# Performance work log

Measured on AMD Instinct MI355X. Metric: run time of the kernel, lower is better.

Reference implementation:

```python
import jax, jax.numpy as jnp
import numpy as np

IN_FEATURES = 128
OUT_FEATURES = 128
GRID_SIZE = 5
SPLINE_ORDER = 3
N_KNOTS = GRID_SIZE + 2 * SPLINE_ORDER + 1  # 12
N_BASIS = GRID_SIZE + SPLINE_ORDER          # 8


def b_spline_basis(x, grid, spline_order):
    # x: [N, in], grid: [in, n_knots] -> basis: [N, in, n_basis]
    xe = x[..., None]
    basis = ((xe >= grid[..., :-1]) & (xe < grid[..., 1:])).astype(x.dtype)
    for k in range(1, spline_order + 1):
        left = (xe - grid[..., :-(k + 1)]) / (grid[..., k:-1] - grid[..., :-(k + 1)] + 1e-08)
        right = (grid[..., k + 1:] - xe) / (grid[..., k + 1:] - grid[..., 1:-k] + 1e-08)
        basis = left * basis[..., :-1] + right * basis[..., 1:]
    return basis


def setup_inputs() -> dict:
    key = jax.random.key(0)
    k_x, k_bw, k_sw = jax.random.split(key, 3)
    x = jax.random.normal(k_x, (16, 4096, IN_FEATURES), dtype=jnp.float32)
    grid = jnp.tile(jnp.linspace(-1.0, 1.0, N_KNOTS, dtype=jnp.float32)[None, :], (IN_FEATURES, 1))
    base_weight = jax.random.normal(k_bw, (OUT_FEATURES, IN_FEATURES), dtype=jnp.float32) * 0.1
    base_bias = jnp.zeros((OUT_FEATURES,), dtype=jnp.float32)
    spline_weight = jax.random.normal(k_sw, (OUT_FEATURES, IN_FEATURES, N_BASIS), dtype=jnp.float32) * 0.1
    spline_bias = jnp.zeros((OUT_FEATURES,), dtype=jnp.float32)
    spline_scale = jnp.ones((1,), dtype=jnp.float32)
    return {"x": x, "grid": grid, "base_weight": base_weight, "base_bias": base_bias,
            "spline_weight": spline_weight, "spline_bias": spline_bias, "spline_scale": spline_scale}


def reference(x, grid, base_weight, base_bias, spline_weight, spline_bias, spline_scale):
    orig_shape = x.shape
    x_flat = x.reshape(-1, IN_FEATURES)                      # [N, in]
    base_out = jax.nn.silu(x_flat) @ base_weight.T + base_bias  # [N, out]
    x_norm = jnp.tanh(x_flat)
    basis = b_spline_basis(x_norm, grid, SPLINE_ORDER)       # [N, in, n_basis]
    spline_out = jnp.einsum('oib,nib->no', spline_weight, basis) + spline_bias
    out = base_out + spline_scale * spline_out
    return out.reshape(*orig_shape[:-1], OUT_FEATURES)
```

## Files before the change

kernel.cpp:

```cpp
#include <hip/hip_runtime.h>
#include <hip/hip_bf16.h>


typedef __attribute__((ext_vector_type(8))) short short8;
typedef __attribute__((ext_vector_type(4))) float f32x4;
typedef __attribute__((ext_vector_type(4))) unsigned int u32x4;
typedef __attribute__((ext_vector_type(8))) unsigned short u16x8;

#define GLOAD_LDS16(g, l) __builtin_amdgcn_global_load_lds(                 \
    (const __attribute__((address_space(1))) void*)(g),                     \
    (__attribute__((address_space(3))) void*)(l), 16, 0, 0)

__device__ __forceinline__ unsigned short f2bf(float f) {
    unsigned u = __builtin_bit_cast(unsigned, f);
    return (unsigned short)((u + 0x7fffu + ((u >> 16) & 1u)) >> 16);
}
__device__ __forceinline__ unsigned pack_bf2(float lo, float hi) {
    unsigned r;
    asm("v_cvt_pk_bf16_f32 %0, %1, %2" : "=v"(r) : "v"(lo), "v"(hi));
    return r;
}
__device__ __forceinline__ float fexp2(float f) { return __builtin_amdgcn_exp2f(f); }
__device__ __forceinline__ float frcp(float f)  { return __builtin_amdgcn_rcpf(f); }
__device__ __forceinline__ float fsilu(float v) {
    return v * frcp(1.0f + fexp2(v * -1.442695041f));
}

__device__ __forceinline__ short8 spline_frag(float xv) {
    const float s6 = 0.16666667f;
    float e  = fexp2(xv * 2.885390082f);
    float r  = frcp(1.0f + e);
    float t  = __builtin_fmaf(-2.0f, r, 1.0f);
    float u  = __builtin_fmaf(t, 5.5f, 5.5f);
    int   j  = (int)u;
    float w  = u - (float)j;
    float w2 = w * w;
    float v0 = __builtin_fmaf(__builtin_fmaf(__builtin_fmaf(-s6, w, 0.5f), w, -0.5f), w, s6);
    float v1 = __builtin_fmaf(__builtin_fmaf(0.5f, w, -1.0f), w2, 0.66666667f);
    float v3 = (w * s6) * w2;
    float v2 = (1.0f - v0) - (v1 + v3);
    unsigned P01 = pack_bf2(v0, v1);
    unsigned P23 = pack_bf2(v2, v3);
    unsigned long long P = (unsigned long long)P01 | ((unsigned long long)P23 << 32);
    int s = (j - 3) << 4;
    unsigned long long lo, hi;
    lo = (s >= 0) ? ((s < 64) ? (P << s) : 0ull) : (P >> (-s));
    hi = (s <= 0) ? 0ull
                  : ((s < 64) ? (P >> (64 - s))
                              : ((s < 128) ? (P << (s - 64)) : 0ull));
    u32x4 f = { (unsigned)lo, (unsigned)(lo >> 32), (unsigned)hi, (unsigned)(hi >> 32) };
    return __builtin_bit_cast(short8, f);
}

__global__ void kan_prep(const float* __restrict__ spline_w,
                         const float* __restrict__ base_w,
                         const float* __restrict__ scale_p,
                         unsigned short* __restrict__ wpre) {
    int g   = blockIdx.x * 256 + threadIdx.x;
    int p   = g >> 11;
    int rem = g & 2047;
    int o   = rem >> 4;
    int k0  = (rem & 15) << 3;
    const float* src = (p < 8) ? (spline_w + (o << 10) + (p << 7) + k0)
                               : (base_w + (o << 7) + k0);
    float s = (p < 8) ? scale_p[0] : 1.0f;
    float4 a = *(const float4*)(src);
    float4 b = *(const float4*)(src + 4);
    u16x8 pk = { f2bf(a.x * s), f2bf(a.y * s), f2bf(a.z * s), f2bf(a.w * s),
                 f2bf(b.x * s), f2bf(b.y * s), f2bf(b.z * s), f2bf(b.w * s) };
    unsigned byte = (unsigned)(((o << 8) + (k0 << 1)) ^ ((o & 7) << 4));
    *(u16x8*)((char*)wpre + (p << 15) + byte) = pk;
}

__global__ __launch_bounds__(256, 2) void kan_main(
    const float* __restrict__ x,
    const unsigned short* __restrict__ wpre,
    const float* __restrict__ base_b,
    const float* __restrict__ spline_b,
    const float* __restrict__ scale_p,
    float* __restrict__ out)
{
    __shared__ unsigned short lds_w[2 * 128 * 128];

    const int tid  = threadIdx.x;
    const int lane = tid & 63;
    const int wave = tid >> 6;
    const int l15  = lane & 15;
    const int kb   = lane >> 4;
    const int row0 = (int)blockIdx.x * 128;

    f32x4 acc[2][8];
#pragma unroll
    for (int m = 0; m < 2; ++m)
#pragma unroll
        for (int n = 0; n < 8; ++n) acc[m][n] = (f32x4){0.f, 0.f, 0.f, 0.f};

    char* lwbase = (char*)lds_w;
    const char* wsrc = (const char*)wpre;

    const float* xp0 = x + (row0 + (wave << 5) + l15) * 128 + kb;
    const float* xp1 = xp0 + 16 * 128;

    {
        const char* src = wsrc + (wave << 13) + (lane << 4);
        char* dst = lwbase + (wave << 13);
#pragma unroll
        for (int it = 0; it < 8; ++it) GLOAD_LDS16(src + (it << 10), dst + (it << 10));
    }
    float xsA[2][4], xsB[2][4];
    float4 xb[2][4][2];
#pragma unroll
    for (int ks = 0; ks < 4; ++ks) { xsA[0][ks] = xp0[ks << 2]; xsA[1][ks] = xp1[ks << 2]; }
    __syncthreads();

#define PHASE(P, XS_CUR, XS_NXT)                                              \
    {                                                                         \
        char* cur = lwbase + (((P) & 1) << 15);                               \
        char* nxt = lwbase + ((((P) + 1) & 1) << 15);                         \
        {                                                                     \
            const char* src = wsrc + (((P) + 1) << 15) + (wave << 13) + (lane << 4); \
            char* dst = nxt + (wave << 13);                                   \
            _Pragma("unroll")                                                 \
            for (int it = 0; it < 8; ++it)                                    \
                GLOAD_LDS16(src + (it << 10), dst + (it << 10));              \
        }                                                                     \
        if ((P) < 7) {                                                        \
            const int c = ((P) + 1) << 4;                                     \
            _Pragma("unroll")                                                 \
            for (int ks = 0; ks < 4; ++ks) {                                  \
                XS_NXT[0][ks] = xp0[c + (ks << 2)];                           \
                XS_NXT[1][ks] = xp1[c + (ks << 2)];                           \
            }                                                                 \
        } else {                                                              \
            const float* xq0 = x + (row0 + (wave << 5) + l15) * 128 + (kb << 3); \
            const float* xq1 = xq0 + 16 * 128;                                \
            _Pragma("unroll")                                                 \
            for (int ks = 0; ks < 4; ++ks) {                                  \
                xb[0][ks][0] = *(const float4*)(xq0 + (ks << 5));             \
                xb[0][ks][1] = *(const float4*)(xq0 + (ks << 5) + 4);         \
                xb[1][ks][0] = *(const float4*)(xq1 + (ks << 5));             \
                xb[1][ks][1] = *(const float4*)(xq1 + (ks << 5) + 4);         \
            }                                                                 \
        }                                                                     \
        short8 af[2][4];                                                      \
        _Pragma("unroll")                                                     \
        for (int m = 0; m < 2; ++m)                                           \
            _Pragma("unroll")                                                 \
            for (int ks = 0; ks < 4; ++ks) af[m][ks] = spline_frag(XS_CUR[m][ks]); \
        _Pragma("unroll")                                                     \
        for (int ks = 0; ks < 4; ++ks) {                                      \
            short8 bfr[8];                                                    \
            _Pragma("unroll")                                                 \
            for (int n = 0; n < 8; ++n) {                                     \
                int o = (n << 4) + l15;                                       \
                unsigned byte = (unsigned)(((o << 8) + (ks << 6) + (kb << 4)) ^ ((o & 7) << 4)); \
                bfr[n] = *(const short8*)(cur + byte);                        \
            }                                                                 \
            _Pragma("unroll")                                                 \
            for (int m = 0; m < 2; ++m)                                       \
                _Pragma("unroll")                                             \
                for (int n = 0; n < 8; ++n)                                   \
                    acc[m][n] = __builtin_amdgcn_mfma_f32_16x16x32_bf16(      \
                        af[m][ks], bfr[n], acc[m][n], 0, 0, 0);               \
        }                                                                     \
        __syncthreads();                                                      \
    }

    PHASE(0, xsA, xsB)
    PHASE(1, xsB, xsA)
    PHASE(2, xsA, xsB)
    PHASE(3, xsB, xsA)
    PHASE(4, xsA, xsB)
    PHASE(5, xsB, xsA)
    PHASE(6, xsA, xsB)
    PHASE(7, xsB, xsA)
#undef PHASE

    {
        char* cur = lwbase;
        short8 af[2][4];
#pragma unroll
        for (int m = 0; m < 2; ++m)
#pragma unroll
            for (int ks = 0; ks < 4; ++ks) {
                float4 a0 = xb[m][ks][0], a1 = xb[m][ks][1];
                u32x4 f = { pack_bf2(fsilu(a0.x), fsilu(a0.y)),
                            pack_bf2(fsilu(a0.z), fsilu(a0.w)),
                            pack_bf2(fsilu(a1.x), fsilu(a1.y)),
                            pack_bf2(fsilu(a1.z), fsilu(a1.w)) };
                af[m][ks] = __builtin_bit_cast(short8, f);
            }
#pragma unroll
        for (int ks = 0; ks < 4; ++ks) {
            short8 bfr[8];
#pragma unroll
            for (int n = 0; n < 8; ++n) {
                int o = (n << 4) + l15;
                unsigned byte = (unsigned)(((o << 8) + (ks << 6) + (kb << 4)) ^ ((o & 7) << 4));
                bfr[n] = *(const short8*)(cur + byte);
            }
#pragma unroll
            for (int m = 0; m < 2; ++m)
#pragma unroll
                for (int n = 0; n < 8; ++n)
                    acc[m][n] = __builtin_amdgcn_mfma_f32_16x16x32_bf16(
                        af[m][ks], bfr[n], acc[m][n], 0, 0, 0);
        }
    }

    const float scale = scale_p[0];
    float* ob = out + (row0 + (wave << 5) + (kb << 2)) * 128 + l15;
#pragma unroll
    for (int n = 0; n < 8; ++n) {
        int o = (n << 4) + l15;
        float bias = base_b[o] + scale * spline_b[o];
#pragma unroll
        for (int m = 0; m < 2; ++m) {
            float* obm = ob + (m << 4) * 128 + (n << 4);
#pragma unroll
            for (int j = 0; j < 4; ++j)
                obm[j * 128] = acc[m][n][j] + bias;
        }
    }
}

extern "C" void kernel_launch(void* const* d_in, const int* in_sizes, int n_in,
                              void* d_out, int out_size, void* d_ws, size_t ws_size,
                              hipStream_t stream) {
    const float* x  = (const float*)d_in[0];
    const float* bw = (const float*)d_in[2];
    const float* bb = (const float*)d_in[3];
    const float* sw = (const float*)d_in[4];
    const float* sb = (const float*)d_in[5];
    const float* sc = (const float*)d_in[6];
    float* out = (float*)d_out;

    unsigned short* wpre = (unsigned short*)d_ws;
    hipLaunchKernelGGL(kan_prep, dim3(72), dim3(256), 0, stream, sw, bw, sc, wpre);

    int nrows   = in_sizes[0] / 128;
    int nblocks = nrows / 128;
    hipLaunchKernelGGL(kan_main, dim3(nblocks), dim3(256), 0, stream,
                       x, wpre, bb, sb, sc, out);
}
```

Baseline: 42.26 us.

## Software-pipeline spline basis computation one phase ahead, interleaved with MFMAs

Computes the A-fragments (spline basis or SiLU) for the next phase while the current phase's MFMAs run, spreading the VALU work between MFMA groups rather than doing it all before them. X loads now run two phases ahead, with a double-buffered fragment array. The goal is to overlap VALU transcendental work with matrix-core execution. In exchange it raises register pressure (two fragment sets plus two x buffers), which could lower occupancy or cause spills.

```diff
diff --git a/kernel.cpp b/kernel.cpp
--- a/kernel.cpp
+++ b/kernel.cpp
@@ -109,11 +109,18 @@
     }
     float xsA[2][4], xsB[2][4];
     float4 xb[2][4][2];
+    short8 afA[2][4], afB[2][4];
 #pragma unroll
     for (int ks = 0; ks < 4; ++ks) { xsA[0][ks] = xp0[ks << 2]; xsA[1][ks] = xp1[ks << 2]; }
+#pragma unroll
+    for (int ks = 0; ks < 4; ++ks) { xsB[0][ks] = xp0[16 + (ks << 2)]; xsB[1][ks] = xp1[16 + (ks << 2)]; }
+#pragma unroll
+    for (int m = 0; m < 2; ++m)
+#pragma unroll
+        for (int ks = 0; ks < 4; ++ks) afA[m][ks] = spline_frag(xsA[m][ks]);
     __syncthreads();
 
-#define PHASE(P, XS_CUR, XS_NXT)                                              \
+#define PHASE(P, XS_CONS, XS_LOAD, AF_CUR, AF_NXT)                            \
     {                                                                         \
         char* cur = lwbase + (((P) & 1) << 15);                               \
         char* nxt = lwbase + ((((P) + 1) & 1) << 15);                         \
@@ -124,14 +131,14 @@
             for (int it = 0; it < 8; ++it)                                    \
                 GLOAD_LDS16(src + (it << 10), dst + (it << 10));              \
         }                                                                     \
-        if ((P) < 7) {                                                        \
-            const int c = ((P) + 1) << 4;                                     \
+        if ((P) < 6) {                                                        \
+            const int c = ((P) + 2) << 4;                                     \
             _Pragma("unroll")                                                 \
             for (int ks = 0; ks < 4; ++ks) {                                  \
-                XS_NXT[0][ks] = xp0[c + (ks << 2)];                           \
-                XS_NXT[1][ks] = xp1[c + (ks << 2)];                           \
-            }                                                                 \
-        } else {                                                              \
+                XS_LOAD[0][ks] = xp0[c + (ks << 2)];                          \
+                XS_LOAD[1][ks] = xp1[c + (ks << 2)];                          \
+            }                                                                 \
+        } else if ((P) == 6) {                                                \
             const float* xq0 = x + (row0 + (wave << 5) + l15) * 128 + (kb << 3); \
             const float* xq1 = xq0 + 16 * 128;                                \
             _Pragma("unroll")                                                 \
@@ -142,11 +149,6 @@
                 xb[1][ks][1] = *(const float4*)(xq1 + (ks << 5) + 4);         \
             }                                                                 \
         }                                                                     \
-        short8 af[2][4];                                                      \
-        _Pragma("unroll")                                                     \
-        for (int m = 0; m < 2; ++m)                                           \
-            _Pragma("unroll")                                                 \
-            for (int ks = 0; ks < 4; ++ks) af[m][ks] = spline_frag(XS_CUR[m][ks]); \
         _Pragma("unroll")                                                     \
         for (int ks = 0; ks < 4; ++ks) {                                      \
             short8 bfr[8];                                                    \
@@ -157,39 +159,41 @@
                 bfr[n] = *(const short8*)(cur + byte);                        \
             }                                                                 \
             _Pragma("unroll")                                                 \
+            for (int e = 0; e < 2; ++e) {                                     \
+                const int q = (ks << 1) + e, fm = q >> 2, fk = q & 3;         \
+                if ((P) < 7) {                                                \
+                    AF_NXT[fm][fk] = spline_frag(XS_CONS[fm][fk]);            \
+                } else {                                                      \
+                    float4 a0 = xb[fm][fk][0], a1 = xb[fm][fk][1];            \
+                    u32x4 f = { pack_bf2(fsilu(a0.x), fsilu(a0.y)),           \
+                                pack_bf2(fsilu(a0.z), fsilu(a0.w)),           \
+                                pack_bf2(fsilu(a1.x), fsilu(a1.y)),           \
+                                pack_bf2(fsilu(a1.z), fsilu(a1.w)) };         \
+                    AF_NXT[fm][fk] = __builtin_bit_cast(short8, f);           \
+                }                                                             \
+            }                                                                 \
+            _Pragma("unroll")                                                 \
             for (int m = 0; m < 2; ++m)                                       \
                 _Pragma("unroll")                                             \
                 for (int n = 0; n < 8; ++n)                                   \
                     acc[m][n] = __builtin_amdgcn_mfma_f32_16x16x32_bf16(      \
-                        af[m][ks], bfr[n], acc[m][n], 0, 0, 0);               \
+                        AF_CUR[m][ks], bfr[n], acc[m][n], 0, 0, 0);           \
         }                                                                     \
         __syncthreads();                                                      \
     }
 
-    PHASE(0, xsA, xsB)
-    PHASE(1, xsB, xsA)
-    PHASE(2, xsA, xsB)
-    PHASE(3, xsB, xsA)
-    PHASE(4, xsA, xsB)
-    PHASE(5, xsB, xsA)
-    PHASE(6, xsA, xsB)
-    PHASE(7, xsB, xsA)
+    PHASE(0, xsB, xsA, afA, afB)
+    PHASE(1, xsA, xsB, afB, afA)
+    PHASE(2, xsB, xsA, afA, afB)
+    PHASE(3, xsA, xsB, afB, afA)
+    PHASE(4, xsB, xsA, afA, afB)
+    PHASE(5, xsA, xsB, afB, afA)
+    PHASE(6, xsB, xsA, afA, afB)
+    PHASE(7, xsA, xsB, afB, afA)
 #undef PHASE
 
     {
         char* cur = lwbase;
-        short8 af[2][4];
-#pragma unroll
-        for (int m = 0; m < 2; ++m)
-#pragma unroll
-            for (int ks = 0; ks < 4; ++ks) {
-                float4 a0 = xb[m][ks][0], a1 = xb[m][ks][1];
-                u32x4 f = { pack_bf2(fsilu(a0.x), fsilu(a0.y)),
-                            pack_bf2(fsilu(a0.z), fsilu(a0.w)),
-                            pack_bf2(fsilu(a1.x), fsilu(a1.y)),
-                            pack_bf2(fsilu(a1.z), fsilu(a1.w)) };
-                af[m][ks] = __builtin_bit_cast(short8, f);
-            }
 #pragma unroll
         for (int ks = 0; ks < 4; ++ks) {
             short8 bfr[8];
@@ -204,7 +208,7 @@
 #pragma unroll
                 for (int n = 0; n < 8; ++n)
                     acc[m][n] = __builtin_amdgcn_mfma_f32_16x16x32_bf16(
-                        af[m][ks], bfr[n], acc[m][n], 0, 0, 0);
+                        afA[m][ks], bfr[n], acc[m][n], 0, 0, 0);
         }
     }
 
```

Result: slower. 61.80 us (+46.3%).

## Halve row tile and K-stage size to raise occupancy to four blocks per CU

Applied to the files above, without the earlier changes.

The main kernel now processes 64 rows per block (one 16-row M tile per wave) instead of 128, and splits each weight stage into half-K chunks of 64, giving 18 stages of 16KB LDS instead of 9 stages of 32KB. The prep kernel relayouts weights into the matching 64-wide swizzled chunks, and launch bounds rise to 4 blocks per CU. The aim is more resident waves and more blocks to hide latency, at the cost of twice as many barriers, reloading weights per block twice as often, and less B-fragment reuse per LDS read.

```diff
diff --git a/kernel.cpp b/kernel.cpp
--- a/kernel.cpp
+++ b/kernel.cpp
@@ -57,22 +57,22 @@
                          const float* __restrict__ scale_p,
                          unsigned short* __restrict__ wpre) {
     int g   = blockIdx.x * 256 + threadIdx.x;
-    int p   = g >> 11;
-    int rem = g & 2047;
-    int o   = rem >> 4;
-    int k0  = (rem & 15) << 3;
-    const float* src = (p < 8) ? (spline_w + (o << 10) + (p << 7) + k0)
-                               : (base_w + (o << 7) + k0);
-    float s = (p < 8) ? scale_p[0] : 1.0f;
+    int hp  = g >> 10;
+    int rem = g & 1023;
+    int o   = rem >> 3;
+    int k0  = (rem & 7) << 3;
+    const float* src = (hp < 16) ? (spline_w + (o << 10) + (hp << 6) + k0)
+                                 : (base_w + (o << 7) + ((hp - 16) << 6) + k0);
+    float s = (hp < 16) ? scale_p[0] : 1.0f;
     float4 a = *(const float4*)(src);
     float4 b = *(const float4*)(src + 4);
     u16x8 pk = { f2bf(a.x * s), f2bf(a.y * s), f2bf(a.z * s), f2bf(a.w * s),
                  f2bf(b.x * s), f2bf(b.y * s), f2bf(b.z * s), f2bf(b.w * s) };
-    unsigned byte = (unsigned)(((o << 8) + (k0 << 1)) ^ ((o & 7) << 4));
-    *(u16x8*)((char*)wpre + (p << 15) + byte) = pk;
-}
-
-__global__ __launch_bounds__(256, 2) void kan_main(
+    unsigned byte = (unsigned)(((o << 7) + (k0 << 1)) ^ ((o & 7) << 4));
+    *(u16x8*)((char*)wpre + (hp << 14) + byte) = pk;
+}
+
+__global__ __launch_bounds__(256, 4) void kan_main(
     const float* __restrict__ x,
     const unsigned short* __restrict__ wpre,
     const float* __restrict__ base_b,
@@ -80,147 +80,144 @@
     const float* __restrict__ scale_p,
     float* __restrict__ out)
 {
-    __shared__ unsigned short lds_w[2 * 128 * 128];
+    __shared__ unsigned short lds_w[2 * 64 * 128];
 
     const int tid  = threadIdx.x;
     const int lane = tid & 63;
     const int wave = tid >> 6;
     const int l15  = lane & 15;
     const int kb   = lane >> 4;
-    const int row0 = (int)blockIdx.x * 128;
-
-    f32x4 acc[2][8];
-#pragma unroll
-    for (int m = 0; m < 2; ++m)
-#pragma unroll
-        for (int n = 0; n < 8; ++n) acc[m][n] = (f32x4){0.f, 0.f, 0.f, 0.f};
+    const int row0 = (int)blockIdx.x * 64;
+    const int row  = row0 + (wave << 4) + l15;
+
+    f32x4 acc[8];
+#pragma unroll
+    for (int n = 0; n < 8; ++n) acc[n] = (f32x4){0.f, 0.f, 0.f, 0.f};
 
     char* lwbase = (char*)lds_w;
     const char* wsrc = (const char*)wpre;
-
-    const float* xp0 = x + (row0 + (wave << 5) + l15) * 128 + kb;
-    const float* xp1 = xp0 + 16 * 128;
+    const float* xp = x + row * 128;
 
     {
-        const char* src = wsrc + (wave << 13) + (lane << 4);
-        char* dst = lwbase + (wave << 13);
-#pragma unroll
-        for (int it = 0; it < 8; ++it) GLOAD_LDS16(src + (it << 10), dst + (it << 10));
-    }
-    float xsA[2][4], xsB[2][4];
-    float4 xb[2][4][2];
-#pragma unroll
-    for (int ks = 0; ks < 4; ++ks) { xsA[0][ks] = xp0[ks << 2]; xsA[1][ks] = xp1[ks << 2]; }
+        const char* src = wsrc + (wave << 12) + (lane << 4);
+        char* dst = lwbase + (wave << 12);
+#pragma unroll
+        for (int it = 0; it < 4; ++it) GLOAD_LDS16(src + (it << 10), dst + (it << 10));
+    }
+    float xsA[2], xsB[2];
+    float4 xb0[2][2], xb1[2][2];
+    xsA[0] = xp[kb];
+    xsA[1] = xp[4 + kb];
     __syncthreads();
 
-#define PHASE(P, XS_CUR, XS_NXT)                                              \
+#define BREAD_MFMA(P_CUR, AF)                                                 \
     {                                                                         \
-        char* cur = lwbase + (((P) & 1) << 15);                               \
-        char* nxt = lwbase + ((((P) + 1) & 1) << 15);                         \
-        {                                                                     \
-            const char* src = wsrc + (((P) + 1) << 15) + (wave << 13) + (lane << 4); \
-            char* dst = nxt + (wave << 13);                                   \
-            _Pragma("unroll")                                                 \
-            for (int it = 0; it < 8; ++it)                                    \
-                GLOAD_LDS16(src + (it << 10), dst + (it << 10));              \
-        }                                                                     \
-        if ((P) < 7) {                                                        \
-            const int c = ((P) + 1) << 4;                                     \
-            _Pragma("unroll")                                                 \
-            for (int ks = 0; ks < 4; ++ks) {                                  \
-                XS_NXT[0][ks] = xp0[c + (ks << 2)];                           \
-                XS_NXT[1][ks] = xp1[c + (ks << 2)];                           \
-            }                                                                 \
-        } else {                                                              \
-            const float* xq0 = x + (row0 + (wave << 5) + l15) * 128 + (kb << 3); \
-            const float* xq1 = xq0 + 16 * 128;                                \
-            _Pragma("unroll")                                                 \
-            for (int ks = 0; ks < 4; ++ks) {                                  \
-                xb[0][ks][0] = *(const float4*)(xq0 + (ks << 5));             \
-                xb[0][ks][1] = *(const float4*)(xq0 + (ks << 5) + 4);         \
-                xb[1][ks][0] = *(const float4*)(xq1 + (ks << 5));             \
-                xb[1][ks][1] = *(const float4*)(xq1 + (ks << 5) + 4);         \
-            }                                                                 \
-        }                                                                     \
-        short8 af[2][4];                                                      \
+        char* cur = lwbase + (((P_CUR) & 1) << 14);                           \
         _Pragma("unroll")                                                     \
-        for (int m = 0; m < 2; ++m)                                           \
-            _Pragma("unroll")                                                 \
-            for (int ks = 0; ks < 4; ++ks) af[m][ks] = spline_frag(XS_CUR[m][ks]); \
-        _Pragma("unroll")                                                     \
-        for (int ks = 0; ks < 4; ++ks) {                                      \
+        for (int ks = 0; ks < 2; ++ks) {                                      \
             short8 bfr[8];                                                    \
             _Pragma("unroll")                                                 \
             for (int n = 0; n < 8; ++n) {                                     \
                 int o = (n << 4) + l15;                                       \
-                unsigned byte = (unsigned)(((o << 8) + (ks << 6) + (kb << 4)) ^ ((o & 7) << 4)); \
+                unsigned byte = (unsigned)(((o << 7) + (ks << 6) + (kb << 4)) \
+                                           ^ ((o & 7) << 4));                 \
                 bfr[n] = *(const short8*)(cur + byte);                        \
             }                                                                 \
             _Pragma("unroll")                                                 \
-            for (int m = 0; m < 2; ++m)                                       \
-                _Pragma("unroll")                                             \
-                for (int n = 0; n < 8; ++n)                                   \
-                    acc[m][n] = __builtin_amdgcn_mfma_f32_16x16x32_bf16(      \
-                        af[m][ks], bfr[n], acc[m][n], 0, 0, 0);               \
+            for (int n = 0; n < 8; ++n)                                       \
+                acc[n] = __builtin_amdgcn_mfma_f32_16x16x32_bf16(             \
+                    AF[ks], bfr[n], acc[n], 0, 0, 0);                         \
         }                                                                     \
-        __syncthreads();                                                      \
-    }
-
-    PHASE(0, xsA, xsB)
-    PHASE(1, xsB, xsA)
-    PHASE(2, xsA, xsB)
-    PHASE(3, xsB, xsA)
-    PHASE(4, xsA, xsB)
-    PHASE(5, xsB, xsA)
-    PHASE(6, xsA, xsB)
-    PHASE(7, xsB, xsA)
-#undef PHASE
+    }
+
+#define STAGE(PN)                                                             \
+    {                                                                         \
+        const char* src = wsrc + ((PN) << 14) + (wave << 12) + (lane << 4);   \
+        char* dst = lwbase + (((PN) & 1) << 14) + (wave << 12);               \
+        _Pragma("unroll")                                                     \
+        for (int it = 0; it < 4; ++it)                                        \
+            GLOAD_LDS16(src + (it << 10), dst + (it << 10));                  \
+    }
+
+    for (int hp = 0; hp < 16; hp += 2) {
+        {
+            const int P = hp;
+            STAGE(P + 1)
+            xsB[0] = xp[((P + 1) << 3) + kb];
+            xsB[1] = xp[((P + 1) << 3) + 4 + kb];
+            short8 af[2];
+            af[0] = spline_frag(xsA[0]);
+            af[1] = spline_frag(xsA[1]);
+            BREAD_MFMA(P, af)
+            __syncthreads();
+        }
+        {
+            const int P = hp + 1;
+            STAGE(P + 1)
+            if (P < 15) {
+                xsA[0] = xp[((P + 1) << 3) + kb];
+                xsA[1] = xp[((P + 1) << 3) + 4 + kb];
+            } else {
+#pragma unroll
+                for (int ks = 0; ks < 2; ++ks) {
+                    xb0[ks][0] = *(const float4*)(xp + (ks << 5) + (kb << 3));
+                    xb0[ks][1] = *(const float4*)(xp + (ks << 5) + (kb << 3) + 4);
+                }
+            }
+            short8 af[2];
+            af[0] = spline_frag(xsB[0]);
+            af[1] = spline_frag(xsB[1]);
+            BREAD_MFMA(P, af)
+            __syncthreads();
+        }
+    }
 
     {
-        char* cur = lwbase;
-        short8 af[2][4];
-#pragma unroll
-        for (int m = 0; m < 2; ++m)
-#pragma unroll
-            for (int ks = 0; ks < 4; ++ks) {
-                float4 a0 = xb[m][ks][0], a1 = xb[m][ks][1];
-                u32x4 f = { pack_bf2(fsilu(a0.x), fsilu(a0.y)),
-                            pack_bf2(fsilu(a0.z), fsilu(a0.w)),
-                            pack_bf2(fsilu(a1.x), fsilu(a1.y)),
-                            pack_bf2(fsilu(a1.z), fsilu(a1.w)) };
-                af[m][ks] = __builtin_bit_cast(short8, f);
-            }
-#pragma unroll
-        for (int ks = 0; ks < 4; ++ks) {
-            short8 bfr[8];
-#pragma unroll
-            for (int n = 0; n < 8; ++n) {
-                int o = (n << 4) + l15;
-                unsigned byte = (unsigned)(((o << 8) + (ks << 6) + (kb << 4)) ^ ((o & 7) << 4));
-                bfr[n] = *(const short8*)(cur + byte);
-            }
-#pragma unroll
-            for (int m = 0; m < 2; ++m)
-#pragma unroll
-                for (int n = 0; n < 8; ++n)
-                    acc[m][n] = __builtin_amdgcn_mfma_f32_16x16x32_bf16(
-                        af[m][ks], bfr[n], acc[m][n], 0, 0, 0);
-        }
-    }
+        STAGE(17)
+#pragma unroll
+        for (int ks = 0; ks < 2; ++ks) {
+            xb1[ks][0] = *(const float4*)(xp + 64 + (ks << 5) + (kb << 3));
+            xb1[ks][1] = *(const float4*)(xp + 64 + (ks << 5) + (kb << 3) + 4);
+        }
+        short8 af[2];
+#pragma unroll
+        for (int ks = 0; ks < 2; ++ks) {
+            float4 a0 = xb0[ks][0], a1 = xb0[ks][1];
+            u32x4 f = { pack_bf2(fsilu(a0.x), fsilu(a0.y)),
+                        pack_bf2(fsilu(a0.z), fsilu(a0.w)),
+                        pack_bf2(fsilu(a1.x), fsilu(a1.y)),
+                        pack_bf2(fsilu(a1.z), fsilu(a1.w)) };
+            af[ks] = __builtin_bit_cast(short8, f);
+        }
+        BREAD_MFMA(16, af)
+        __syncthreads();
+    }
+    {
+        short8 af[2];
+#pragma unroll
+        for (int ks = 0; ks < 2; ++ks) {
+            float4 a0 = xb1[ks][0], a1 = xb1[ks][1];
+            u32x4 f = { pack_bf2(fsilu(a0.x), fsilu(a0.y)),
+                        pack_bf2(fsilu(a0.z), fsilu(a0.w)),
+                        pack_bf2(fsilu(a1.x), fsilu(a1.y)),
+                        pack_bf2(fsilu(a1.z), fsilu(a1.w)) };
+            af[ks] = __builtin_bit_cast(short8, f);
+        }
+        BREAD_MFMA(17, af)
+    }
+#undef BREAD_MFMA
+#undef STAGE
 
     const float scale = scale_p[0];
-    float* ob = out + (row0 + (wave << 5) + (kb << 2)) * 128 + l15;
+    float* ob = out + (row0 + (wave << 4) + (kb << 2)) * 128 + l15;
 #pragma unroll
     for (int n = 0; n < 8; ++n) {
         int o = (n << 4) + l15;
         float bias = base_b[o] + scale * spline_b[o];
-#pragma unroll
-        for (int m = 0; m < 2; ++m) {
-            float* obm = ob + (m << 4) * 128 + (n << 4);
-#pragma unroll
-            for (int j = 0; j < 4; ++j)
-                obm[j * 128] = acc[m][n][j] + bias;
-        }
+        float* obm = ob + (n << 4);
+#pragma unroll
+        for (int j = 0; j < 4; ++j)
+            obm[j * 128] = acc[n][j] + bias;
     }
 }
 
@@ -239,7 +236,7 @@
     hipLaunchKernelGGL(kan_prep, dim3(72), dim3(256), 0, stream, sw, bw, sc, wpre);
 
     int nrows   = in_sizes[0] / 128;
-    int nblocks = nrows / 128;
+    int nblocks = nrows / 64;
     hipLaunchKernelGGL(kan_main, dim3(nblocks), dim3(256), 0, stream,
                        x, wpre, bb, sb, sc, out);
 }
```

Measured after the change: 44.05 us. +4.2%, slower.

## Keep weight fragments resident in registers and loop over row tiles per block

Applied to the files above, without the earlier changes.

Each wave now loads its 32-output slice of the bf16 weights (spline plus base, 72 short8 fragments) from global into VGPRs once. It then loops over 8 row tiles of 32 rows, which removes the LDS double-buffer staging, the per-phase barriers and the LDS fragment reads. The prep kernel re-lays out weights as per-output rows of 2304 bytes in an order matching the new K ordering. Each block handles 256 rows, so there are half as many blocks, and launch bounds drop to 1 block per CU. This costs heavy register pressure (possible spills), lower occupancy, and per-tile x loads that are no longer prefetched.

```diff
diff --git a/kernel.cpp b/kernel.cpp
--- a/kernel.cpp
+++ b/kernel.cpp
@@ -6,10 +6,6 @@
 typedef __attribute__((ext_vector_type(4))) float f32x4;
 typedef __attribute__((ext_vector_type(4))) unsigned int u32x4;
 typedef __attribute__((ext_vector_type(8))) unsigned short u16x8;
-
-#define GLOAD_LDS16(g, l) __builtin_amdgcn_global_load_lds(                 \
-    (const __attribute__((address_space(1))) void*)(g),                     \
-    (__attribute__((address_space(3))) void*)(l), 16, 0, 0)
 
 __device__ __forceinline__ unsigned short f2bf(float f) {
     unsigned u = __builtin_bit_cast(unsigned, f);
@@ -56,23 +52,28 @@
                          const float* __restrict__ base_w,
                          const float* __restrict__ scale_p,
                          unsigned short* __restrict__ wpre) {
-    int g   = blockIdx.x * 256 + threadIdx.x;
-    int p   = g >> 11;
-    int rem = g & 2047;
-    int o   = rem >> 4;
-    int k0  = (rem & 15) << 3;
-    const float* src = (p < 8) ? (spline_w + (o << 10) + (p << 7) + k0)
-                               : (base_w + (o << 7) + k0);
-    float s = (p < 8) ? scale_p[0] : 1.0f;
-    float4 a = *(const float4*)(src);
-    float4 b = *(const float4*)(src + 4);
-    u16x8 pk = { f2bf(a.x * s), f2bf(a.y * s), f2bf(a.z * s), f2bf(a.w * s),
-                 f2bf(b.x * s), f2bf(b.y * s), f2bf(b.z * s), f2bf(b.w * s) };
-    unsigned byte = (unsigned)(((o << 8) + (k0 << 1)) ^ ((o & 7) << 4));
-    *(u16x8*)((char*)wpre + (p << 15) + byte) = pk;
+    int g  = blockIdx.x * 256 + threadIdx.x;
+    int o  = g / 144;
+    int k0 = (g % 144) << 3;
+    const float* src;
+    float s;
+    if (k0 < 1024) {
+        int ks = k0 >> 5, kb = (k0 >> 3) & 3;
+        int fi = (kb << 5) + ks;
+        src = spline_w + (o << 10) + (fi << 3);
+        s = scale_p[0];
+    } else {
+        src = base_w + (o << 7) + (k0 - 1024);
+        s = 1.0f;
+    }
+    f32x4 a = *(const f32x4*)(src);
+    f32x4 b = *(const f32x4*)(src + 4);
+    u16x8 pk = { f2bf(a[0] * s), f2bf(a[1] * s), f2bf(a[2] * s), f2bf(a[3] * s),
+                 f2bf(b[0] * s), f2bf(b[1] * s), f2bf(b[2] * s), f2bf(b[3] * s) };
+    *(u16x8*)((char*)wpre + o * 2304 + (k0 << 1)) = pk;
 }
 
-__global__ __launch_bounds__(256, 2) void kan_main(
+__global__ __launch_bounds__(256, 1) void kan_main(
     const float* __restrict__ x,
     const unsigned short* __restrict__ wpre,
     const float* __restrict__ base_b,
@@ -80,147 +81,74 @@
     const float* __restrict__ scale_p,
     float* __restrict__ out)
 {
-    __shared__ unsigned short lds_w[2 * 128 * 128];
-
     const int tid  = threadIdx.x;
     const int lane = tid & 63;
-    const int wave = tid >> 6;
+    const int wq   = tid >> 6;
     const int l15  = lane & 15;
     const int kb   = lane >> 4;
-    const int row0 = (int)blockIdx.x * 128;
+    const int row_blk = (int)blockIdx.x << 8;
 
-    f32x4 acc[2][8];
+    const char* wp = (const char*)wpre + ((wq << 5) + l15) * 2304 + (kb << 4);
+    short8 B0[36], B1[36];
 #pragma unroll
-    for (int m = 0; m < 2; ++m)
+    for (int t = 0; t < 36; ++t) B0[t] = *(const short8*)(wp + (t << 6));
 #pragma unroll
-        for (int n = 0; n < 8; ++n) acc[m][n] = (f32x4){0.f, 0.f, 0.f, 0.f};
+    for (int t = 0; t < 36; ++t) B1[t] = *(const short8*)(wp + 36864 + (t << 6));
 
-    char* lwbase = (char*)lds_w;
-    const char* wsrc = (const char*)wpre;
+    const float scale = scale_p[0];
+    const int o0 = (wq << 5) + l15;
+    const float bias0 = base_b[o0] + scale * spline_b[o0];
+    const float bias1 = base_b[o0 + 16] + scale * spline_b[o0 + 16];
 
-    const float* xp0 = x + (row0 + (wave << 5) + l15) * 128 + kb;
-    const float* xp1 = xp0 + 16 * 128;
+    for (int tile = 0; tile < 8; ++tile) {
+        const int r0 = row_blk + (tile << 5);
+        f32x4 acc[2][2];
+#pragma unroll
+        for (int m = 0; m < 2; ++m) {
+            acc[m][0] = (f32x4){0.f, 0.f, 0.f, 0.f};
+            acc[m][1] = (f32x4){0.f, 0.f, 0.f, 0.f};
+        }
 
-    {
-        const char* src = wsrc + (wave << 13) + (lane << 4);
-        char* dst = lwbase + (wave << 13);
 #pragma unroll
-        for (int it = 0; it < 8; ++it) GLOAD_LDS16(src + (it << 10), dst + (it << 10));
-    }
-    float xsA[2][4], xsB[2][4];
-    float4 xb[2][4][2];
+        for (int m = 0; m < 2; ++m) {
+            const float* xr = x + (r0 + (m << 4) + l15) * 128;
+            f32x4 xs[8];
 #pragma unroll
-    for (int ks = 0; ks < 4; ++ks) { xsA[0][ks] = xp0[ks << 2]; xsA[1][ks] = xp1[ks << 2]; }
-    __syncthreads();
+            for (int c = 0; c < 8; ++c)
+                xs[c] = *(const f32x4*)(xr + (kb << 5) + (c << 2));
+            f32x4 xb[8];
+#pragma unroll
+            for (int c = 0; c < 8; ++c)
+                xb[c] = *(const f32x4*)(xr + ((c >> 1) << 5) + (kb << 3) + ((c & 1) << 2));
 
-#define PHASE(P, XS_CUR, XS_NXT)                                              \
-    {                                                                         \
-        char* cur = lwbase + (((P) & 1) << 15);                               \
-        char* nxt = lwbase + ((((P) + 1) & 1) << 15);                         \
-        {                                                                     \
-            const char* src = wsrc + (((P) + 1) << 15) + (wave << 13) + (lane << 4); \
-            char* dst = nxt + (wave << 13);                                   \
-            _Pragma("unroll")                                                 \
-            for (int it = 0; it < 8; ++it)                                    \
-                GLOAD_LDS16(src + (it << 10), dst + (it << 10));              \
-        }                                                                     \
-        if ((P) < 7) {                                                        \
-            const int c = ((P) + 1) << 4;                                     \
-            _Pragma("unroll")                                                 \
-            for (int ks = 0; ks < 4; ++ks) {                                  \
-                XS_NXT[0][ks] = xp0[c + (ks << 2)];                           \
-                XS_NXT[1][ks] = xp1[c + (ks << 2)];                           \
-            }                                                                 \
-        } else {                                                              \
-            const float* xq0 = x + (row0 + (wave << 5) + l15) * 128 + (kb << 3); \
-            const float* xq1 = xq0 + 16 * 128;                                \
-            _Pragma("unroll")                                                 \
-            for (int ks = 0; ks < 4; ++ks) {                                  \
-                xb[0][ks][0] = *(const float4*)(xq0 + (ks << 5));             \
-                xb[0][ks][1] = *(const float4*)(xq0 + (ks << 5) + 4);         \
-                xb[1][ks][0] = *(const float4*)(xq1 + (ks << 5));             \
-                xb[1][ks][1] = *(const float4*)(xq1 + (ks << 5) + 4);         \
-            }                                                                 \
-        }                                                                     \
-        short8 af[2][4];                                                      \
-        _Pragma("unroll")                                                     \
-        for (int m = 0; m < 2; ++m)                                           \
-            _Pragma("unroll")                                                 \
-            for (int ks = 0; ks < 4; ++ks) af[m][ks] = spline_frag(XS_CUR[m][ks]); \
-        _Pragma("unroll")                                                     \
-        for (int ks = 0; ks < 4; ++ks) {                                      \
-            short8 bfr[8];                                                    \
-            _Pragma("unroll")                                                 \
-            for (int n = 0; n < 8; ++n) {                                     \
-                int o = (n << 4) + l15;                                       \
-                unsigned byte = (unsigned)(((o << 8) + (ks << 6) + (kb << 4)) ^ ((o & 7) << 4)); \
-                bfr[n] = *(const short8*)(cur + byte);                        \
-            }                                                                 \
-            _Pragma("unroll")                                                 \
-            for (int m = 0; m < 2; ++m)                                       \
-                _Pragma("unroll")                                             \
-                for (int n = 0; n < 8; ++n)                                   \
-                    acc[m][n] = __builtin_amdgcn_mfma_f32_16x16x32_bf16(      \
-                        af[m][ks], bfr[n], acc[m][n], 0, 0, 0);               \
-        }                                                                     \
-        __syncthreads();                                                      \
-    }
+#pragma unroll
+            for (int ks = 0; ks < 32; ++ks) {
+                short8 af = spline_frag(xs[ks >> 2][ks & 3]);
+                acc[m][0] = __builtin_amdgcn_mfma_f32_16x16x32_bf16(af, B0[ks], acc[m][0], 0, 0, 0);
+                acc[m][1] = __builtin_amdgcn_mfma_f32_16x16x32_bf16(af, B1[ks], acc[m][1], 0, 0, 0);
+            }
+#pragma unroll
+            for (int s = 0; s < 4; ++s) {
+                f32x4 p = xb[s << 1], q = xb[(s << 1) + 1];
+                u32x4 f = { pack_bf2(fsilu(p[0]), fsilu(p[1])),
+                            pack_bf2(fsilu(p[2]), fsilu(p[3])),
+                            pack_bf2(fsilu(q[0]), fsilu(q[1])),
+                            pack_bf2(fsilu(q[2]), fsilu(q[3])) };
+                short8 af = __builtin_bit_cast(short8, f);
+                acc[m][0] = __builtin_amdgcn_mfma_f32_16x16x32_bf16(af, B0[32 + s], acc[m][0], 0, 0, 0);
+                acc[m][1] = __builtin_amdgcn_mfma_f32_16x16x32_bf16(af, B1[32 + s], acc[m][1], 0, 0, 0);
+            }
+        }
 
-    PHASE(0, xsA, xsB)
-    PHASE(1, xsB, xsA)
-    PHASE(2, xsA, xsB)
-    PHASE(3, xsB, xsA)
-    PHASE(4, xsA, xsB)
-    PHASE(5, xsB, xsA)
-    PHASE(6, xsA, xsB)
-    PHASE(7, xsB, xsA)
-#undef PHASE
-
-    {
-        char* cur = lwbase;
-        short8 af[2][4];
+        float* ob = out + (r0 + (kb << 2)) * 128 + o0;
 #pragma unroll
         for (int m = 0; m < 2; ++m)
 #pragma unroll
-            for (int ks = 0; ks < 4; ++ks) {
-                float4 a0 = xb[m][ks][0], a1 = xb[m][ks][1];
-                u32x4 f = { pack_bf2(fsilu(a0.x), fsilu(a0.y)),
-                            pack_bf2(fsilu(a0.z), fsilu(a0.w)),
-                            pack_bf2(fsilu(a1.x), fsilu(a1.y)),
-                            pack_bf2(fsilu(a1.z), fsilu(a1.w)) };
-                af[m][ks] = __builtin_bit_cast(short8, f);
+            for (int j = 0; j < 4; ++j) {
+                float* orow = ob + ((m << 4) + j) * 128;
+                orow[0]  = acc[m][0][j] + bias0;
+                orow[16] = acc[m][1][j] + bias1;
             }
-#pragma unroll
-        for (int ks = 0; ks < 4; ++ks) {
-            short8 bfr[8];
-#pragma unroll
-            for (int n = 0; n < 8; ++n) {
-                int o = (n << 4) + l15;
-                unsigned byte = (unsigned)(((o << 8) + (ks << 6) + (kb << 4)) ^ ((o & 7) << 4));
-                bfr[n] = *(const short8*)(cur + byte);
-            }
-#pragma unroll
-            for (int m = 0; m < 2; ++m)
-#pragma unroll
-                for (int n = 0; n < 8; ++n)
-                    acc[m][n] = __builtin_amdgcn_mfma_f32_16x16x32_bf16(
-                        af[m][ks], bfr[n], acc[m][n], 0, 0, 0);
-        }
-    }
-
-    const float scale = scale_p[0];
-    float* ob = out + (row0 + (wave << 5) + (kb << 2)) * 128 + l15;
-#pragma unroll
-    for (int n = 0; n < 8; ++n) {
-        int o = (n << 4) + l15;
-        float bias = base_b[o] + scale * spline_b[o];
-#pragma unroll
-        for (int m = 0; m < 2; ++m) {
-            float* obm = ob + (m << 4) * 128 + (n << 4);
-#pragma unroll
-            for (int j = 0; j < 4; ++j)
-                obm[j * 128] = acc[m][n][j] + bias;
-        }
     }
 }
 
@@ -239,7 +167,7 @@
     hipLaunchKernelGGL(kan_prep, dim3(72), dim3(256), 0, stream, sw, bw, sc, wpre);
 
     int nrows   = in_sizes[0] / 128;
-    int nblocks = nrows / 128;
+    int nblocks = nrows / 256;
     hipLaunchKernelGGL(kan_main, dim3(nblocks), dim3(256), 0, stream,
                        x, wpre, bb, sb, sc, out);
 }
```

Result: slower. 102.5 us (+142.6%).
